# Kernel optimization log

Hardware: AMD Instinct MI355X
Metric: run time of the kernel (lower is better)

## Reference

```python
import jax, jax.numpy as jnp
import numpy as np

T = 2048          # tokens (single-sequence prefill)
HID = 4096        # hidden_size
NH = 32           # num attention heads
NKV = 8           # num kv heads (GQA)
HD = 128          # head_dim
QKV_OUT = (NH + 2 * NKV) * HD  # 6144
THETA = 10000.0
SCALING = HD ** -0.5


def setup_inputs() -> dict:
    key = jax.random.key(0)
    ks = jax.random.split(key, 8)
    positions = jnp.arange(T, dtype=jnp.int32)
    # per-token int8 quantized hidden states (symmetric, [-127,127])
    q_act = jax.random.randint(ks[0], (T, HID), -127, 128, dtype=jnp.int32)
    # per-token dynamic activation scale
    act_scale = jax.random.uniform(ks[1], (T,), jnp.float32) * 0.01 + 0.001
    # int4 weights stored unsigned [0,15] with per-output-channel scale & zero point
    w_qkv_q = jax.random.randint(ks[2], (QKV_OUT, HID), 0, 16, dtype=jnp.int32)
    w_qkv_scale = jax.random.uniform(ks[3], (QKV_OUT,), jnp.float32) * 0.01 + 0.001
    w_qkv_zero = jax.random.uniform(ks[4], (QKV_OUT,), jnp.float32) * 2.0 + 7.0
    w_o_q = jax.random.randint(ks[5], (HID, HID), 0, 16, dtype=jnp.int32)
    w_o_scale = jax.random.uniform(ks[6], (HID,), jnp.float32) * 0.01 + 0.001
    w_o_zero = jax.random.uniform(ks[7], (HID,), jnp.float32) * 2.0 + 7.0
    return dict(positions=positions, q_act=q_act, act_scale=act_scale,
                w_qkv_q=w_qkv_q, w_qkv_scale=w_qkv_scale, w_qkv_zero=w_qkv_zero,
                w_o_q=w_o_q, w_o_scale=w_o_scale, w_o_zero=w_o_zero)


def w4a8_linear(qa_f, s_a, a_sum, qw, s_w, z_w):
    # y[t,o] = s_a[t]*s_w[o] * ( (qa @ qw^T)[t,o] - z_w[o]*sum_j qa[t,j] )
    acc = jnp.matmul(qa_f, qw.astype(jnp.float32).T)  # [T, O]
    return (s_a[:, None] * s_w[None, :]) * (acc - z_w[None, :] * a_sum[:, None])


def apply_rope(x, positions):
    # neox-style RoPE over full head_dim
    half = HD // 2
    inv_freq = THETA ** (-jnp.arange(0, half, dtype=jnp.float32) / half * 1.0)
    inv_freq = 1.0 / (THETA ** (jnp.arange(0, HD, 2, dtype=jnp.float32) / HD))
    freqs = positions.astype(jnp.float32)[:, None] * inv_freq[None, :]  # [T, HD/2]
    cos = jnp.cos(freqs)[:, None, :]
    sin = jnp.sin(freqs)[:, None, :]
    x1, x2 = x[..., :half], x[..., half:]
    return jnp.concatenate([x1 * cos - x2 * sin, x2 * cos + x1 * sin], axis=-1)


def dynamic_quant_with_sum(x):
    # per-token symmetric int8 dynamic quantization + fused sum
    s = jnp.maximum(jnp.max(jnp.abs(x), axis=-1), 1e-8) / 127.0  # [T]
    q = jnp.clip(jnp.round(x / s[:, None]), -127, 127)
    return q, s, jnp.sum(q, axis=-1)


def reference(positions, q_act, act_scale, w_qkv_q, w_qkv_scale, w_qkv_zero,
              w_o_q, w_o_scale, w_o_zero):
    qa_f = q_act.astype(jnp.float32)
    a_sum = jnp.sum(qa_f, axis=-1)  # fused activation sum
    qkv = w4a8_linear(qa_f, act_scale, a_sum, w_qkv_q, w_qkv_scale, w_qkv_zero)
    q, k, v = jnp.split(qkv, [NH * HD, NH * HD + NKV * HD], axis=-1)
    q = q.reshape(T, NH, HD)
    k = k.reshape(T, NKV, HD)
    v = v.reshape(T, NKV, HD)
    q = apply_rope(q, positions)
    k = apply_rope(k, positions)
    # GQA: repeat kv heads
    rep = NH // NKV
    k = jnp.repeat(k, rep, axis=1)  # [T, NH, HD]
    v = jnp.repeat(v, rep, axis=1)
    scores = jnp.einsum('qhd,khd->hqk', q, k) * SCALING  # [NH, T, T]
    causal = jnp.tril(jnp.ones((T, T), dtype=bool))
    scores = jnp.where(causal[None], scores, -jnp.inf)
    probs = jax.nn.softmax(scores, axis=-1)
    attn = jnp.einsum('hqk,khd->qhd', probs, v).reshape(T, NH * HD)
    # invoke_quant_fuse_sum: dynamic per-token quantization of attn output
    q2, s2, sum2 = dynamic_quant_with_sum(attn)
    out = w4a8_linear(q2, s2, sum2, w_o_q, w_o_scale, w_o_zero)
    return out
```

## Files before the change

### kernel.cpp

```cpp
#include <hip/hip_runtime.h>

#define T 2048
#define HID 4096
#define NH 32
#define NKV 8
#define HD 128
#define QKV_OUT ((NH + 2*NKV) * HD)
#define SCALING 0.08838834764831843f
#define QS2 0.12751744954f
#define DEFER_THR 10.0f
#define ROPE_C 0.20762050593046014f

typedef __attribute__((ext_vector_type(8))) short bfrag;
typedef __attribute__((ext_vector_type(4))) float ffrag;
typedef __attribute__((ext_vector_type(4))) int  ifrag;
typedef __attribute__((ext_vector_type(16))) char c16;

__device__ __forceinline__ short f2bf(float f) {
  unsigned u = __builtin_bit_cast(unsigned, f);
  u += 0x7fffu + ((u >> 16) & 1u);
  return (short)(u >> 16);
}

__device__ __forceinline__ void split2(float x, short& hi, short& lo) {
  unsigned u = __builtin_bit_cast(unsigned, x);
  unsigned uh = u + (0x7fffu + ((u >> 16) & 1u));
  hi = (short)(uh >> 16);
  float fh = __builtin_bit_cast(float, uh & 0xffff0000u);
  float r = x - fh;
  unsigned ur = __builtin_bit_cast(unsigned, r);
  ur += 0x7fffu + ((ur >> 16) & 1u);
  lo = (short)(ur >> 16);
}

__device__ __forceinline__ void gload_lds16(const void* g, void* l) {
  __builtin_amdgcn_global_load_lds(
      (const __attribute__((address_space(1))) unsigned int*)g,
      (__attribute__((address_space(3))) unsigned int*)l, 16, 0, 0);
}

__global__ __launch_bounds__(256)
void rope_table(float2* __restrict__ tab) {
  int idx = blockIdx.x * 256 + threadIdx.x;
  int p = idx >> 6, j = idx & 63;
  float fr = (float)p * exp2f(-ROPE_C * (float)j);
  float sn, cs; sincosf(fr, &sn, &cs);
  tab[idx] = make_float2(cs, sn);
}


__global__ __launch_bounds__(256)
void asum_conv(const int* __restrict__ qact, float* __restrict__ a_sum,
               char* __restrict__ a_i8) {
  __shared__ int red[256];
  const int t = blockIdx.x, tid = threadIdx.x;
  const int* row = qact + (size_t)t * HID + tid * 16;
  int s = 0;
  c16 o;
#pragma unroll
  for (int i = 0; i < 4; i++) {
    int4 v = *(const int4*)(row + i * 4);
    s += v.x + v.y + v.z + v.w;
    o[i*4+0] = (char)v.x; o[i*4+1] = (char)v.y;
    o[i*4+2] = (char)v.z; o[i*4+3] = (char)v.w;
  }
  const int chunk = (tid & ~7) | ((tid & 7) ^ (t & 7));
  *(c16*)(a_i8 + (size_t)t * HID + chunk * 16) = o;
  red[tid] = s; __syncthreads();
  for (int off = 128; off > 0; off >>= 1) {
    if (tid < off) red[tid] += red[tid + off];
    __syncthreads();
  }
  if (tid == 0) a_sum[t] = (float)red[0];
}

__global__ __launch_bounds__(256)
void conv_i2c(const int* __restrict__ src, char* __restrict__ dst, int n16) {
  int idx = blockIdx.x * 256 + threadIdx.x;
  if (idx >= n16) return;
  const int4* s4 = (const int4*)src + (size_t)idx * 4;
  c16 o;
#pragma unroll
  for (int j = 0; j < 4; j++) {
    int4 v = s4[j];
    o[j*4+0] = (char)v.x; o[j*4+1] = (char)v.y;
    o[j*4+2] = (char)v.z; o[j*4+3] = (char)v.w;
  }
  const int idxp = (idx & ~7) | ((idx & 7) ^ ((idx >> 8) & 7));
  *(c16*)(dst + (size_t)idxp * 16) = o;
}

__global__ __launch_bounds__(256)
void gemm_i8(const char* __restrict__ A, const char* __restrict__ W,
             const float* __restrict__ s_a, const float* __restrict__ asum,
             const float* __restrict__ s_w, const float* __restrict__ z_w,
             float* __restrict__ C, int M, int N, int K) {
  __shared__ __align__(16) char As[2][128 * 128];
  __shared__ __align__(16) char Bs[2][128 * 128];
  const int tid = threadIdx.x;
  const int lane = tid & 63;
  const int quad = lane >> 4, l15 = lane & 15;
  const int wave = tid >> 6;
  const int wm = (wave >> 1) * 64, wn = (wave & 1) * 64;
  const int bm = blockIdx.y * 128, bn = blockIdx.x * 128;
  const int sr = tid >> 3, sc = (tid & 7) * 16;

  ifrag acc[4][4];
#pragma unroll
  for (int mi = 0; mi < 4; mi++)
#pragma unroll
    for (int ni = 0; ni < 4; ni++)
      acc[mi][ni] = (ifrag){0, 0, 0, 0};

  auto stage = [&](int k0, int b) {
#pragma unroll
    for (int j = 0; j < 4; j++) {
      gload_lds16(A + (size_t)(bm + j * 32 + sr) * K + k0 + sc,
                  &As[b][j * 4096 + tid * 16]);
      gload_lds16(W + (size_t)(bn + j * 32 + sr) * K + k0 + sc,
                  &Bs[b][j * 4096 + tid * 16]);
    }
  };

  const int scol0 = ((quad)     ^ (l15 & 7)) * 16;
  const int scol1 = ((4 + quad) ^ (l15 & 7)) * 16;

  stage(0, 0);
  asm volatile("s_waitcnt vmcnt(0)" ::: "memory");
  __builtin_amdgcn_s_barrier();

  int cur = 0;
  for (int k0 = 0; k0 < K; k0 += 128) {
    if (k0 + 128 < K) stage(k0 + 128, cur ^ 1);

#pragma unroll
    for (int ks = 0; ks < 2; ks++) {
      const int scol = ks ? scol1 : scol0;
      ifrag af[4], bfv[4];
#pragma unroll
      for (int mi = 0; mi < 4; mi++)
        af[mi] = *(const ifrag*)&As[cur][(wm + mi * 16 + l15) * 128 + scol];
#pragma unroll
      for (int ni = 0; ni < 4; ni++)
        bfv[ni] = *(const ifrag*)&Bs[cur][(wn + ni * 16 + l15) * 128 + scol];
#pragma unroll
      for (int mi = 0; mi < 4; mi++)
#pragma unroll
        for (int ni = 0; ni < 4; ni++)
          acc[mi][ni] = __builtin_amdgcn_mfma_i32_16x16x64_i8(
              af[mi], bfv[ni], acc[mi][ni], 0, 0, 0);
    }

    asm volatile("s_waitcnt vmcnt(0)" ::: "memory");
    __builtin_amdgcn_s_barrier();
    cur ^= 1;
  }

#pragma unroll
  for (int mi = 0; mi < 4; mi++) {
    int row0 = bm + wm + mi * 16 + quad * 4;
#pragma unroll
    for (int r = 0; r < 4; r++) {
      int row = row0 + r;
      float sa = s_a[row], av = asum[row];
#pragma unroll
      for (int ni = 0; ni < 4; ni++) {
        int col = bn + wn + ni * 16 + l15;
        C[(size_t)row * N + col] = (sa * s_w[col]) * ((float)acc[mi][ni][r] - z_w[col] * av);
      }
    }
  }
}

__global__ __launch_bounds__(256)
void split_kv(float* __restrict__ qkv, const int* __restrict__ positions,
              const float2* __restrict__ tab,
              short* __restrict__ Kh, short* __restrict__ Kl,
              short* __restrict__ Vth) {
  __shared__ __align__(16) short Vh_lds[128 * 72];
  const int y = blockIdx.y;
  const int t0 = blockIdx.x * 64;
  const int tid = threadIdx.x;

  if (y >= NKV) {
    const int h = y - NKV;
#pragma unroll
    for (int it = 0; it < 4; it++) {
      int c = tid + 256 * it;
      int key = c >> 4, dc = c & 15;
      float* qr = qkv + (size_t)(t0 + key) * QKV_OUT + (size_t)h * HD;
      float4 a = *(const float4*)(qr + dc * 4);
      float4 b = *(const float4*)(qr + dc * 4 + 64);
      float av[4] = {a.x, a.y, a.z, a.w};
      float bv[4] = {b.x, b.y, b.z, b.w};
      const float2* tr = tab + (size_t)positions[t0 + key] * 64 + dc * 4;
#pragma unroll
      for (int jj = 0; jj < 4; jj++) {
        float cs = tr[jj].x, sn = tr[jj].y;
        float x1 = av[jj], x2 = bv[jj];
        av[jj] = x1 * cs - x2 * sn;
        bv[jj] = x2 * cs + x1 * sn;
      }
      *(float4*)(qr + dc * 4)      = make_float4(av[0], av[1], av[2], av[3]);
      *(float4*)(qr + dc * 4 + 64) = make_float4(bv[0], bv[1], bv[2], bv[3]);
    }
    return;
  }

  const int kvh = y;
#pragma unroll
  for (int it = 0; it < 4; it++) {
    int c = tid + 256 * it;
    int key = c >> 4, dc = c & 15;
    const int t = t0 + key;
    const float* kr = qkv + (size_t)t * QKV_OUT
                      + (size_t)NH * HD + (size_t)kvh * HD;
    float4 a = *(const float4*)(kr + dc * 4);
    float4 b = *(const float4*)(kr + dc * 4 + 64);
    float av[4] = {a.x, a.y, a.z, a.w};
    float bv[4] = {b.x, b.y, b.z, b.w};
    const float2* tr = tab + (size_t)positions[t] * 64 + dc * 4;
    short4 ha, la, hb, lb;
    short hh, ll;
#pragma unroll
    for (int jj = 0; jj < 4; jj++) {
      float cs = tr[jj].x, sn = tr[jj].y;
      float x1 = av[jj], x2 = bv[jj];
      float r1 = x1 * cs - x2 * sn;
      float r2 = x2 * cs + x1 * sn;
      split2(r1, hh, ll); ((short*)&ha)[jj] = hh; ((short*)&la)[jj] = ll;
      split2(r2, hh, ll); ((short*)&hb)[jj] = hh; ((short*)&lb)[jj] = ll;
    }
    const int uu = ((dc >> 1) ^ t) & 7;
    const int h4 = (dc & 1) * 4;
    size_t base = (size_t)kvh * T * HD + (size_t)t * HD;
    *(short4*)(Kh + base + uu * 8 + h4) = ha;
    *(short4*)(Kl + base + uu * 8 + h4) = la;
    *(short4*)(Kh + base + (8 + uu) * 8 + h4) = hb;
    *(short4*)(Kl + base + (8 + uu) * 8 + h4) = lb;
  }
#pragma unroll
  for (int i = 0; i < 8; i++) {
    int c = tid + 256 * i;
    int key = c >> 5, dc = c & 31;
    float4 f = *(const float4*)(qkv + (size_t)(t0 + key) * QKV_OUT
                                + (size_t)(NH + NKV) * HD + (size_t)kvh * HD + dc * 4);
    Vh_lds[(dc*4+0)*72 + key] = f2bf(f.x);
    Vh_lds[(dc*4+1)*72 + key] = f2bf(f.y);
    Vh_lds[(dc*4+2)*72 + key] = f2bf(f.z);
    Vh_lds[(dc*4+3)*72 + key] = f2bf(f.w);
  }
  __syncthreads();
#pragma unroll
  for (int i = 0; i < 2; i++) {
    int c = tid + 256 * i;
    int row = c >> 2, cc = c & 3;
    int sd = (row >> 1) & 3;
    size_t o = (size_t)kvh * HD * T + (size_t)row * T + t0 + ((cc ^ sd)) * 8;
    *(bfrag*)(Vth + o) = *(const bfrag*)&Vh_lds[row * 72 + cc * 8];
  }
#pragma unroll
  for (int i = 0; i < 2; i++) {
    int c = tid + 256 * i;
    int row = c >> 2, cc = c & 3;
    int sd = (row >> 1) & 3;
    size_t o = (size_t)kvh * HD * T + (size_t)row * T + t0 + 32 + ((cc ^ sd)) * 8;
    *(bfrag*)(Vth + o) = *(const bfrag*)&Vh_lds[row * 72 + 32 + cc * 8];
  }
}

__global__ __launch_bounds__(256)
void attn_kernel(const float* __restrict__ qkv,
                 const short* __restrict__ Kh, const short* __restrict__ Kl,
                 const short* __restrict__ Vth,
                 float* __restrict__ attn) {
  __shared__ __align__(16) short Ksh[2][32 * 128];
  __shared__ __align__(16) short Ksl[2][32 * 128];
  __shared__ __align__(16) short Vsh[2][128 * 32];
  __shared__ __align__(16) short Psh[4 * 16 * 40];

  const int kvh = blockIdx.x & 7;
  const int pair = blockIdx.x >> 3;
  const int tid = threadIdx.x;
  const int lane = tid & 63;
  const int wv = tid >> 6;
  const int l15 = lane & 15, quad = lane >> 4;
  const int h = kvh * 4 + wv;
  short* Pw = Psh + wv * 16 * 40;

  const short* KhB = Kh + (size_t)kvh * T * HD;
  const short* KlB = Kl + (size_t)kvh * T * HD;
  const short* VhB = Vth + (size_t)kvh * HD * T;

  const int offK0 = (tid >> 4) * 128 + (tid & 15) * 8;
  const int offK1 = offK0 + 16 * 128;
  const int offV0 = (tid >> 2) * T + (tid & 3) * 8;
  const int offV1 = offV0 + 64 * T;
  const int wv1k = wv * 1024;

  auto stage = [&](int k0, int b) {
    const short* khs = KhB + (size_t)k0 * HD;
    const short* kls = KlB + (size_t)k0 * HD;
    const short* vs  = VhB + k0;
    gload_lds16(khs + offK0, (char*)&Ksh[b][0] + wv1k);
    gload_lds16(khs + offK1, (char*)&Ksh[b][0] + 4096 + wv1k);
    gload_lds16(kls + offK0, (char*)&Ksl[b][0] + wv1k);
    gload_lds16(kls + offK1, (char*)&Ksl[b][0] + 4096 + wv1k);
    gload_lds16(vs + offV0, (char*)&Vsh[b][0] + wv1k);
    gload_lds16(vs + offV1, (char*)&Vsh[b][0] + 4096 + wv1k);
  };

  const int sdv = (l15 >> 1) & 3;
  const int vq8 = (quad ^ sdv) * 8;
  int uuk[4];
#pragma unroll
  for (int kc = 0; kc < 4; kc++) {
    int s = 4 * kc + quad;
    uuk[kc] = ((s & 8) | ((s ^ l15) & 7)) * 8;
  }

  bfrag ones;
#pragma unroll
  for (int j = 0; j < 8; j++) ones[j] = (short)0x3f80;

  for (int pass = 0; pass < 2; pass++) {
    const int qt = pass ? pair : 127 - pair;
    const int q0 = qt * 16;
    const int nk = (q0 >> 5) + 1;

    bfrag qh[4], ql[4];
    const float* qrow = qkv + (size_t)(q0 + l15) * QKV_OUT + (size_t)h * HD;
#pragma unroll
    for (int kc = 0; kc < 4; kc++) {
      float4 f0 = *(const float4*)(qrow + kc * 32 + quad * 8);
      float4 f1 = *(const float4*)(qrow + kc * 32 + quad * 8 + 4);
      float fv[8] = {f0.x, f0.y, f0.z, f0.w, f1.x, f1.y, f1.z, f1.w};
#pragma unroll
      for (int j = 0; j < 8; j++) {
        short hi, lo; split2(fv[j] * QS2, hi, lo);
        qh[kc][j] = hi; ql[kc][j] = lo;
      }
    }

    ffrag o[8], ol;
    ol = (ffrag){0.f, 0.f, 0.f, 0.f};
#pragma unroll
    for (int n = 0; n < 8; n++) o[n] = (ffrag){0.f, 0.f, 0.f, 0.f};
    float m_i[4] = {-1e30f, -1e30f, -1e30f, -1e30f};

    stage(0, 0);
    asm volatile("s_waitcnt vmcnt(0)" ::: "memory");
    __builtin_amdgcn_s_barrier();

    int cur = 0;
    for (int kt = 0; kt < nk; kt++) {
      const int k0 = kt << 5;
      if (kt + 1 < nk) stage(k0 + 32, cur ^ 1);

      const short* ksh = &Ksh[cur][0];
      const short* ksl = &Ksl[cur][0];
      const short* vsh = &Vsh[cur][0];

      ffrag s[2];
      s[0] = (ffrag){0.f,0.f,0.f,0.f}; s[1] = (ffrag){0.f,0.f,0.f,0.f};
#pragma unroll
      for (int kc = 0; kc < 4; kc++) {
#pragma unroll
        for (int n = 0; n < 2; n++) {
          const int rb = (n * 16 + l15) * 128 + uuk[kc];
          bfrag bh = *(const bfrag*)&ksh[rb];
          bfrag bl = *(const bfrag*)&ksl[rb];
          s[n] = __builtin_amdgcn_mfma_f32_16x16x32_bf16(qh[kc], bh, s[n], 0,0,0);
          s[n] = __builtin_amdgcn_mfma_f32_16x16x32_bf16(qh[kc], bl, s[n], 0,0,0);
          s[n] = __builtin_amdgcn_mfma_f32_16x16x32_bf16(ql[kc], bh, s[n], 0,0,0);
        }
      }
      const bool lastkt = (kt == nk - 1);
      float sv[2][4];
#pragma unroll
      for (int n = 0; n < 2; n++)
#pragma unroll
        for (int r = 0; r < 4; r++) {
          float v = s[n][r];
          if (lastkt) {
            int key = k0 + n * 16 + l15;
            int row = q0 + quad * 4 + r;
            if (key > row) v = -1e30f;
          }
          sv[n][r] = v;
        }
      float lm[4];
      bool trig = false;
#pragma unroll
      for (int r = 0; r < 4; r++) {
        lm[r] = fmaxf(sv[0][r], sv[1][r]);
        trig = trig || (lm[r] > m_i[r] + DEFER_THR);
      }
      if (__any(trig)) {
#pragma unroll
        for (int r = 0; r < 4; r++) {
          float m2 = lm[r];
          m2 = fmaxf(m2, __shfl_xor(m2, 1));
          m2 = fmaxf(m2, __shfl_xor(m2, 2));
          m2 = fmaxf(m2, __shfl_xor(m2, 4));
          m2 = fmaxf(m2, __shfl_xor(m2, 8));
          float mn = fmaxf(m_i[r], m2);
          float a = exp2f(m_i[r] - mn);
          m_i[r] = mn;
          ol[r] *= a;
#pragma unroll
          for (int n = 0; n < 8; n++) o[n][r] *= a;
        }
      }
#pragma unroll
      for (int n = 0; n < 2; n++)
#pragma unroll
        for (int r = 0; r < 4; r++) {
          float p = exp2f(sv[n][r] - m_i[r]);
          Pw[(quad*4 + r) * 40 + n*16 + l15] = f2bf(p);
        }
      bfrag ph = *(const bfrag*)&Pw[l15 * 40 + quad * 8];
      ol = __builtin_amdgcn_mfma_f32_16x16x32_bf16(ph, ones, ol, 0,0,0);
#pragma unroll
      for (int n = 0; n < 8; n++) {
        bfrag vh = *(const bfrag*)&vsh[(n * 16 + l15) * 32 + vq8];
        o[n] = __builtin_amdgcn_mfma_f32_16x16x32_bf16(ph, vh, o[n], 0,0,0);
      }

      asm volatile("s_waitcnt vmcnt(0)" ::: "memory");
      __builtin_amdgcn_s_barrier();
      cur ^= 1;
    }

    float inv[4];
#pragma unroll
    for (int r = 0; r < 4; r++) inv[r] = 1.f / ol[r];
#pragma unroll
    for (int n = 0; n < 8; n++)
#pragma unroll
      for (int r = 0; r < 4; r++) {
        int row = q0 + quad * 4 + r;
        attn[(size_t)row * HID + (size_t)h * HD + n * 16 + l15] = o[n][r] * inv[r];
      }
  }
}

__global__ __launch_bounds__(256)
void quant_kernel(const float* __restrict__ x, char* __restrict__ q2,
                  float* __restrict__ s2, float* __restrict__ sum2) {
  __shared__ float red[256];
  const int t = blockIdx.x, tid = threadIdx.x;
  const float* row = x + (size_t)t * HID;
  float4 v[4];
  float m = 0.f;
#pragma unroll
  for (int i = 0; i < 4; i++) {
    v[i] = *(const float4*)(row + tid * 16 + i * 4);
    m = fmaxf(m, fmaxf(fmaxf(fabsf(v[i].x), fabsf(v[i].y)),
                       fmaxf(fabsf(v[i].z), fabsf(v[i].w))));
  }
  red[tid] = m; __syncthreads();
  for (int off = 128; off > 0; off >>= 1) {
    if (tid < off) red[tid] = fmaxf(red[tid], red[tid + off]);
    __syncthreads();
  }
  float s = fmaxf(red[0], 1e-8f) / 127.f;
  __syncthreads();
  float ssum = 0.f;
  c16 o;
#pragma unroll
  for (int i = 0; i < 4; i++) {
    float q;
    q = fminf(127.f, fmaxf(-127.f, rintf(v[i].x / s))); ssum += q; o[i*4+0] = (char)(int)q;
    q = fminf(127.f, fmaxf(-127.f, rintf(v[i].y / s))); ssum += q; o[i*4+1] = (char)(int)q;
    q = fminf(127.f, fmaxf(-127.f, rintf(v[i].z / s))); ssum += q; o[i*4+2] = (char)(int)q;
    q = fminf(127.f, fmaxf(-127.f, rintf(v[i].w / s))); ssum += q; o[i*4+3] = (char)(int)q;
  }
  const int chunk = (tid & ~7) | ((tid & 7) ^ (t & 7));
  *(c16*)(q2 + (size_t)t * HID + chunk * 16) = o;
  red[tid] = ssum; __syncthreads();
  for (int off = 128; off > 0; off >>= 1) {
    if (tid < off) red[tid] += red[tid + off];
    __syncthreads();
  }
  if (tid == 0) { s2[t] = s; sum2[t] = red[0]; }
}

extern "C" void kernel_launch(void* const* d_in, const int* in_sizes, int n_in,
                              void* d_out, int out_size, void* d_ws, size_t ws_size,
                              hipStream_t stream) {
  const int*   positions   = (const int*)d_in[0];
  const int*   q_act       = (const int*)d_in[1];
  const float* act_scale   = (const float*)d_in[2];
  const int*   w_qkv_q     = (const int*)d_in[3];
  const float* w_qkv_scale = (const float*)d_in[4];
  const float* w_qkv_zero  = (const float*)d_in[5];
  const int*   w_o_q       = (const int*)d_in[6];
  const float* w_o_scale   = (const float*)d_in[7];
  const float* w_o_zero    = (const float*)d_in[8];
  float* out = (float*)d_out;

  size_t off = 0;
  auto alloc = [&](size_t bytes) -> void* {
    void* p = (char*)d_ws + off;
    off += (bytes + 255) & ~(size_t)255;
    return p;
  };
  float* qkv   = (float*)alloc((size_t)T * QKV_OUT * 4);
  char*  act8  = (char*)alloc((size_t)T * HID);
  char*  w8    = (char*)alloc((size_t)QKV_OUT * HID);
  short* Kh    = (short*)alloc((size_t)NKV * T * HD * 2);
  short* Kl    = (short*)alloc((size_t)NKV * T * HD * 2);
  short* Vth   = (short*)alloc((size_t)NKV * T * HD * 2);
  float* a_sum = (float*)alloc(T * 4);
  float* s2    = (float*)alloc(T * 4);
  float* sum2  = (float*)alloc(T * 4);
  float2* tab  = (float2*)alloc((size_t)T * 64 * 8);
  (void)ws_size;

  rope_table<<<T * 64 / 256, 256, 0, stream>>>(tab);
  asum_conv<<<T, 256, 0, stream>>>(q_act, a_sum, act8);
  conv_i2c<<<(QKV_OUT * HID / 16 + 255) / 256, 256, 0, stream>>>(
      w_qkv_q, w8, QKV_OUT * HID / 16);
  gemm_i8<<<dim3(QKV_OUT / 128, T / 128), 256, 0, stream>>>(
      act8, w8, act_scale, a_sum, w_qkv_scale, w_qkv_zero, qkv, T, QKV_OUT, HID);
  split_kv<<<dim3(T / 64, NKV + NH), 256, 0, stream>>>(
      qkv, positions, tab, Kh, Kl, Vth);
  attn_kernel<<<dim3(512), 256, 0, stream>>>(qkv, Kh, Kl, Vth, out);
  conv_i2c<<<(HID * HID / 16 + 255) / 256, 256, 0, stream>>>(
      w_o_q, w8, HID * HID / 16);
  quant_kernel<<<T, 256, 0, stream>>>(out, act8, s2, sum2);
  gemm_i8<<<dim3(HID / 128, T / 128), 256, 0, stream>>>(
      act8, w8, s2, sum2, w_o_scale, w_o_zero, out, T, HID, HID);
}
```

Measured before the change: 478.1 us.

## Fuse Q RoPE into attention, rope table into asum kernel, peel masked tile

Q-side RoPE now runs in the attention kernel's Q load, and split_kv only handles K/V heads, which removes a read-modify-write pass over the Q portion of the qkv buffer. The rope table computation moves into the first 512 blocks of asum_conv, saving one kernel launch. The attention k-loop peels the last (causal-masked) tile so the steady-state loop has no mask branch. Each attention block does a little more work per query tile, and asum_conv gains divergent extra work in its early blocks.

```diff
diff --git a/kernel.cpp b/kernel.cpp
--- a/kernel.cpp
+++ b/kernel.cpp
@@ -39,21 +39,19 @@
       (__attribute__((address_space(3))) unsigned int*)l, 16, 0, 0);
 }
 
-__global__ __launch_bounds__(256)
-void rope_table(float2* __restrict__ tab) {
-  int idx = blockIdx.x * 256 + threadIdx.x;
-  int p = idx >> 6, j = idx & 63;
-  float fr = (float)p * exp2f(-ROPE_C * (float)j);
-  float sn, cs; sincosf(fr, &sn, &cs);
-  tab[idx] = make_float2(cs, sn);
-}
-
 
 __global__ __launch_bounds__(256)
 void asum_conv(const int* __restrict__ qact, float* __restrict__ a_sum,
-               char* __restrict__ a_i8) {
+               char* __restrict__ a_i8, float2* __restrict__ tab) {
   __shared__ int red[256];
   const int t = blockIdx.x, tid = threadIdx.x;
+  if (t < 512) {
+    int idx = t * 256 + tid;
+    int p = idx >> 6, j = idx & 63;
+    float fr = (float)p * exp2f(-ROPE_C * (float)j);
+    float sn, cs; sincosf(fr, &sn, &cs);
+    tab[idx] = make_float2(cs, sn);
+  }
   const int* row = qact + (size_t)t * HID + tid * 16;
   int s = 0;
   c16 o;
@@ -173,41 +171,15 @@
 }
 
 __global__ __launch_bounds__(256)
-void split_kv(float* __restrict__ qkv, const int* __restrict__ positions,
+void split_kv(const float* __restrict__ qkv, const int* __restrict__ positions,
               const float2* __restrict__ tab,
               short* __restrict__ Kh, short* __restrict__ Kl,
               short* __restrict__ Vth) {
   __shared__ __align__(16) short Vh_lds[128 * 72];
-  const int y = blockIdx.y;
+  const int kvh = blockIdx.y;
   const int t0 = blockIdx.x * 64;
   const int tid = threadIdx.x;
 
-  if (y >= NKV) {
-    const int h = y - NKV;
-#pragma unroll
-    for (int it = 0; it < 4; it++) {
-      int c = tid + 256 * it;
-      int key = c >> 4, dc = c & 15;
-      float* qr = qkv + (size_t)(t0 + key) * QKV_OUT + (size_t)h * HD;
-      float4 a = *(const float4*)(qr + dc * 4);
-      float4 b = *(const float4*)(qr + dc * 4 + 64);
-      float av[4] = {a.x, a.y, a.z, a.w};
-      float bv[4] = {b.x, b.y, b.z, b.w};
-      const float2* tr = tab + (size_t)positions[t0 + key] * 64 + dc * 4;
-#pragma unroll
-      for (int jj = 0; jj < 4; jj++) {
-        float cs = tr[jj].x, sn = tr[jj].y;
-        float x1 = av[jj], x2 = bv[jj];
-        av[jj] = x1 * cs - x2 * sn;
-        bv[jj] = x2 * cs + x1 * sn;
-      }
-      *(float4*)(qr + dc * 4)      = make_float4(av[0], av[1], av[2], av[3]);
-      *(float4*)(qr + dc * 4 + 64) = make_float4(bv[0], bv[1], bv[2], bv[3]);
-    }
-    return;
-  }
-
-  const int kvh = y;
 #pragma unroll
   for (int it = 0; it < 4; it++) {
     int c = tid + 256 * it;
@@ -270,7 +242,8 @@
 }
 
 __global__ __launch_bounds__(256)
-void attn_kernel(const float* __restrict__ qkv,
+void attn_kernel(const float* __restrict__ qkv, const int* __restrict__ positions,
+                 const float2* __restrict__ tab,
                  const short* __restrict__ Kh, const short* __restrict__ Kl,
                  const short* __restrict__ Vth,
                  float* __restrict__ attn) {
@@ -329,17 +302,35 @@
     const int nk = (q0 >> 5) + 1;
 
     bfrag qh[4], ql[4];
-    const float* qrow = qkv + (size_t)(q0 + l15) * QKV_OUT + (size_t)h * HD;
-#pragma unroll
-    for (int kc = 0; kc < 4; kc++) {
-      float4 f0 = *(const float4*)(qrow + kc * 32 + quad * 8);
-      float4 f1 = *(const float4*)(qrow + kc * 32 + quad * 8 + 4);
-      float fv[8] = {f0.x, f0.y, f0.z, f0.w, f1.x, f1.y, f1.z, f1.w};
-#pragma unroll
-      for (int j = 0; j < 8; j++) {
-        short hi, lo; split2(fv[j] * QS2, hi, lo);
-        qh[kc][j] = hi; ql[kc][j] = lo;
-      }
+    {
+      const float* qrow = qkv + (size_t)(q0 + l15) * QKV_OUT + (size_t)h * HD;
+      float fvv[4][8];
+#pragma unroll
+      for (int kc = 0; kc < 4; kc++) {
+        float4 f0 = *(const float4*)(qrow + kc * 32 + quad * 8);
+        float4 f1 = *(const float4*)(qrow + kc * 32 + quad * 8 + 4);
+        fvv[kc][0] = f0.x; fvv[kc][1] = f0.y; fvv[kc][2] = f0.z; fvv[kc][3] = f0.w;
+        fvv[kc][4] = f1.x; fvv[kc][5] = f1.y; fvv[kc][6] = f1.z; fvv[kc][7] = f1.w;
+      }
+      const float2* trw = tab + (size_t)positions[q0 + l15] * 64;
+#pragma unroll
+      for (int kc = 0; kc < 2; kc++) {
+#pragma unroll
+        for (int j = 0; j < 8; j++) {
+          int d = kc * 32 + quad * 8 + j;
+          float2 cssn = trw[d];
+          float x1 = fvv[kc][j], x2 = fvv[kc + 2][j];
+          fvv[kc][j]     = x1 * cssn.x - x2 * cssn.y;
+          fvv[kc + 2][j] = x2 * cssn.x + x1 * cssn.y;
+        }
+      }
+#pragma unroll
+      for (int kc = 0; kc < 4; kc++)
+#pragma unroll
+        for (int j = 0; j < 8; j++) {
+          short hi, lo; split2(fvv[kc][j] * QS2, hi, lo);
+          qh[kc][j] = hi; ql[kc][j] = lo;
+        }
     }
 
     ffrag o[8], ol;
@@ -348,19 +339,10 @@
     for (int n = 0; n < 8; n++) o[n] = (ffrag){0.f, 0.f, 0.f, 0.f};
     float m_i[4] = {-1e30f, -1e30f, -1e30f, -1e30f};
 
-    stage(0, 0);
-    asm volatile("s_waitcnt vmcnt(0)" ::: "memory");
-    __builtin_amdgcn_s_barrier();
-
-    int cur = 0;
-    for (int kt = 0; kt < nk; kt++) {
-      const int k0 = kt << 5;
-      if (kt + 1 < nk) stage(k0 + 32, cur ^ 1);
-
-      const short* ksh = &Ksh[cur][0];
-      const short* ksl = &Ksl[cur][0];
-      const short* vsh = &Vsh[cur][0];
-
+    auto compute_tile = [&](int k0, int b, bool maskq) {
+      const short* ksh = &Ksh[b][0];
+      const short* ksl = &Ksl[b][0];
+      const short* vsh = &Vsh[b][0];
       ffrag s[2];
       s[0] = (ffrag){0.f,0.f,0.f,0.f}; s[1] = (ffrag){0.f,0.f,0.f,0.f};
 #pragma unroll
@@ -375,14 +357,13 @@
           s[n] = __builtin_amdgcn_mfma_f32_16x16x32_bf16(ql[kc], bh, s[n], 0,0,0);
         }
       }
-      const bool lastkt = (kt == nk - 1);
       float sv[2][4];
 #pragma unroll
       for (int n = 0; n < 2; n++)
 #pragma unroll
         for (int r = 0; r < 4; r++) {
           float v = s[n][r];
-          if (lastkt) {
+          if (maskq) {
             int key = k0 + n * 16 + l15;
             int row = q0 + quad * 4 + r;
             if (key > row) v = -1e30f;
@@ -426,11 +407,23 @@
         bfrag vh = *(const bfrag*)&vsh[(n * 16 + l15) * 32 + vq8];
         o[n] = __builtin_amdgcn_mfma_f32_16x16x32_bf16(ph, vh, o[n], 0,0,0);
       }
-
+    };
+
+    stage(0, 0);
+    asm volatile("s_waitcnt vmcnt(0)" ::: "memory");
+    __builtin_amdgcn_s_barrier();
+
+    int cur = 0;
+    for (int kt = 0; kt < nk - 1; kt++) {
+      const int k0 = kt << 5;
+      stage(k0 + 32, cur ^ 1);
+      compute_tile(k0, cur, false);
       asm volatile("s_waitcnt vmcnt(0)" ::: "memory");
       __builtin_amdgcn_s_barrier();
       cur ^= 1;
     }
+    compute_tile((nk - 1) << 5, cur, true);
+    __builtin_amdgcn_s_barrier();
 
     float inv[4];
 #pragma unroll
@@ -518,15 +511,15 @@
   float2* tab  = (float2*)alloc((size_t)T * 64 * 8);
   (void)ws_size;
 
-  rope_table<<<T * 64 / 256, 256, 0, stream>>>(tab);
-  asum_conv<<<T, 256, 0, stream>>>(q_act, a_sum, act8);
+  asum_conv<<<T, 256, 0, stream>>>(q_act, a_sum, act8, tab);
   conv_i2c<<<(QKV_OUT * HID / 16 + 255) / 256, 256, 0, stream>>>(
       w_qkv_q, w8, QKV_OUT * HID / 16);
   gemm_i8<<<dim3(QKV_OUT / 128, T / 128), 256, 0, stream>>>(
       act8, w8, act_scale, a_sum, w_qkv_scale, w_qkv_zero, qkv, T, QKV_OUT, HID);
-  split_kv<<<dim3(T / 64, NKV + NH), 256, 0, stream>>>(
+  split_kv<<<dim3(T / 64, NKV), 256, 0, stream>>>(
       qkv, positions, tab, Kh, Kl, Vth);
-  attn_kernel<<<dim3(512), 256, 0, stream>>>(qkv, Kh, Kl, Vth, out);
+  attn_kernel<<<dim3(512), 256, 0, stream>>>(
+      qkv, positions, tab, Kh, Kl, Vth, out);
   conv_i2c<<<(HID * HID / 16 + 255) / 256, 256, 0, stream>>>(
       w_o_q, w8, HID * HID / 16);
   quant_kernel<<<T, 256, 0, stream>>>(out, act8, s2, sum2);
```

New measurement: 467.0 us. 2.3% less time.
